# Optimization experiments

Measured on AMD Instinct MI355X. Metric: run time of the kernel, lower is better.

## Reference

```python
import jax, jax.numpy as jnp
import numpy as np


def _unfold(x, k):
    # x: [B, C, H, W] -> [B, C, S, L] with S=k*k (row-major patch order), L=H*W
    B, C, H, W = x.shape
    pad = k // 2
    xp = jnp.pad(x, ((0, 0), (0, 0), (pad, pad), (pad, pad)))
    patches = jnp.stack(
        [xp[:, :, r:r + H, c:c + W] for r in range(k) for c in range(k)], axis=2
    )  # [B, C, S, H, W]
    return patches.reshape(B, C, k * k, H * W)


def setup_inputs() -> dict:
    key = jax.random.key(0)
    ks = jax.random.split(key, 8)
    B, C, H, W = 8, 64, 128, 128
    R, Cout = 4, 128
    x = jax.random.normal(ks[0], (B, C, H, W), dtype=jnp.float32)
    gate_w = jax.random.normal(ks[1], (R, C), dtype=jnp.float32) * 0.05   # 1x1 gate conv weight
    gate_b = jax.random.normal(ks[2], (R,), dtype=jnp.float32) * 0.01
    theta = jax.random.normal(ks[3], (R,), dtype=jnp.float32) * 0.5       # learned directions
    raw_sigma_u = jax.random.normal(ks[4], (R,), dtype=jnp.float32) * 0.1
    raw_sigma_s = jax.random.normal(ks[5], (R,), dtype=jnp.float32) * 0.1
    pw_w = jax.random.normal(ks[6], (Cout, R * C), dtype=jnp.float32) * (1.0 / np.sqrt(R * C).astype(np.float32))
    pw_b = jax.random.normal(ks[7], (Cout,), dtype=jnp.float32) * 0.01
    return {"x": x, "gate_w": gate_w, "gate_b": gate_b, "theta": theta,
            "raw_sigma_u": raw_sigma_u, "raw_sigma_s": raw_sigma_s,
            "pw_w": pw_w, "pw_b": pw_b}


def reference(x, gate_w, gate_b, theta, raw_sigma_u, raw_sigma_s, pw_w, pw_b):
    k = 3
    B, C, H, W = x.shape
    R = theta.shape[0]
    S, L = k * k, H * W

    x_un = _unfold(x, k)                                         # [B, C, S, L]

    # 1x1 gate conv + fuzzy softmax over rules
    logits = jnp.einsum('bchw,rc->brhw', x, gate_w) + gate_b[None, :, None, None]
    mu = jax.nn.softmax(logits, axis=1)                          # [B, R, H, W]
    mu_un = _unfold(mu, k)                                       # [B, R, S, L]
    s_center = (k // 2) * k + (k // 2)
    mu_center = mu_un[:, :, s_center:s_center + 1, :]            # [B, R, 1, L]

    # anisotropic Gaussian kernel per rule over integer offsets (row-major)
    grid = np.arange(k, dtype=np.float32) - k // 2
    dy = jnp.asarray(np.repeat(grid, k))                         # [S]
    dx = jnp.asarray(np.tile(grid, k))                           # [S]
    cos_t, sin_t = jnp.cos(theta)[:, None], jnp.sin(theta)[:, None]
    proj_u = cos_t * dx[None, :] + sin_t * dy[None, :]           # [R, S]
    proj_s = -sin_t * dx[None, :] + cos_t * dy[None, :]
    su = (jax.nn.softplus(raw_sigma_u) + 1e-4)[:, None]
    ss = (jax.nn.softplus(raw_sigma_s) + 1e-4)[:, None]
    kern = jnp.exp(-proj_u ** 2 / su ** 2 - proj_s ** 2 / ss ** 2)  # [R, S]

    alpha = mu_center * mu_un * kern[None, :, :, None]           # [B, R, S, L]
    alpha_sum = jnp.maximum(alpha.sum(axis=(1, 2), keepdims=True), 1e-8)
    alpha = alpha / alpha_sum

    agg = jnp.einsum('brsl,bcsl->brcl', alpha, x_un)             # [B, R, C, L]
    agg_flat = agg.reshape(B, R * C, L)
    out = jnp.einsum('bnl,on->bol', agg_flat, pw_w) + pw_b[None, :, None]
    return out.reshape(B, -1, H, W)
```

## Files before the change

kernel.cpp:

```cpp
#include <hip/hip_runtime.h>
#include <math.h>

#define CC 64
#define RR 4
#define HH 128
#define WW 128
#define BB 8
#define COUT 128
#define XST 72
#define ALS 44

typedef __attribute__((ext_vector_type(8))) short short8;
typedef __attribute__((ext_vector_type(4))) float f32x4;
typedef __attribute__((ext_vector_type(2))) float f32x2;

__device__ __forceinline__ unsigned short f2bf(float f) {
  unsigned u = __float_as_uint(f);
  u += 0x7fffu + ((u >> 16) & 1u);
  return (unsigned short)(u >> 16);
}
__device__ __forceinline__ float blo(unsigned u) { return __uint_as_float(u << 16); }
__device__ __forceinline__ float bhi(unsigned u) { return __uint_as_float(u & 0xffff0000u); }
__device__ __forceinline__ int swzx(int cb, int sp) { return cb ^ ((sp >> 3) & 7); }
__device__ __forceinline__ int swza(int cb, int row) { return cb ^ ((row >> 3) & 3); }

__global__ __launch_bounds__(256) void k_pre(const float* __restrict__ theta,
                                             const float* __restrict__ rsu,
                                             const float* __restrict__ rss,
                                             const float* __restrict__ pw,
                                             const float* __restrict__ gw,
                                             float* __restrict__ wkern,
                                             unsigned short* __restrict__ pwb,
                                             unsigned short* __restrict__ gwb) {
  int i = blockIdx.x * 256 + threadIdx.x;
  if (i < COUT * RR * CC) pwb[i] = f2bf(pw[i]);
  if (blockIdx.x == 0 && threadIdx.x < RR * 9) {
    int t = threadIdx.x;
    int r = t / 9, s = t % 9;
    float dy = (float)(s / 3 - 1), dx = (float)(s % 3 - 1);
    float ct = cosf(theta[r]), st = sinf(theta[r]);
    float su = log1pf(expf(rsu[r])) + 1e-4f;
    float sv = log1pf(expf(rss[r])) + 1e-4f;
    float pu = ct * dx + st * dy;
    float ps = -st * dx + ct * dy;
    wkern[t] = expf(-(pu * pu) / (su * su) - (ps * ps) / (sv * sv));
  }
  if (blockIdx.x == 1) {
    #pragma unroll
    for (int k = 0; k < 4; ++k) {
      int j = k * 256 + threadIdx.x;
      gwb[j] = (j < RR * CC) ? f2bf(gw[j]) : (unsigned short)0;
    }
  }
}

__global__ __launch_bounds__(256, 3) void k_fused(const float* __restrict__ x,
                                                  const float* __restrict__ gb,
                                                  const float* __restrict__ wkern,
                                                  const unsigned short* __restrict__ pwb,
                                                  const unsigned short* __restrict__ gwb,
                                                  const float* __restrict__ pb,
                                                  float* __restrict__ out) {
  __shared__ unsigned short xsT[160][XST];
  __shared__ float mus[RR][4][40];
  __shared__ unsigned short alp[64][ALS];
  __shared__ float rsum[RR][64];
  __shared__ __align__(16) unsigned short aggs[32][264];

  int tid = threadIdx.x;
  int raw = blockIdx.x;
  int bid = (raw & 7) * 256 + (raw >> 3);
  int b = bid >> 8;
  int rem = bid & 255;
  int h0 = (rem >> 2) << 1;
  int w0 = (rem & 3) << 5;

  int lane = tid & 63;
  int wv = tid >> 6;
  int lr = lane & 15, lq = lane >> 4;
  int o0 = wv << 5;

  short8 a0r[8], a1r[8];
  {
    const unsigned short* pA = pwb + ((o0 + lr) << 8) + (lq << 3);
    #pragma unroll
    for (int ks = 0; ks < 8; ++ks) {
      a0r[ks] = *(const short8*)(pA + (ks << 5));
      a1r[ks] = *(const short8*)(pA + 4096 + (ks << 5));
    }
  }
  short8 am0 = *(const short8*)(gwb + (lr << 6) + (lq << 3));
  short8 am1 = *(const short8*)(gwb + (lr << 6) + 32 + (lq << 3));
  float4 pbv0 = *(const float4*)&pb[o0 + (lq << 2)];
  float4 pbv1 = *(const float4*)&pb[o0 + 16 + (lq << 2)];
  float gb0 = gb[0], gb1 = gb[1], gb2 = gb[2], gb3 = gb[3];

  #pragma unroll
  for (int k = 0; k < 3; ++k) {
    int item = k * 256 + tid;
    if (item < 640) {
      int c4 = item % 10;
      int rest = item / 10;
      int row = rest & 3, cquad = rest >> 2;
      int c = cquad << 2;
      int gcol = w0 - 4 + (c4 << 2);
      int grow = h0 - 1 + row;
      float4 v0 = make_float4(0.f,0.f,0.f,0.f), v1 = v0, v2 = v0, v3 = v0;
      if ((unsigned)gcol < WW && (unsigned)grow < HH) {
        const float* xp = x + (((size_t)b * CC + c) << 14) + (grow << 7) + gcol;
        v0 = *(const float4*)xp;
        v1 = *(const float4*)(xp + (1 << 14));
        v2 = *(const float4*)(xp + (2 << 14));
        v3 = *(const float4*)(xp + (3 << 14));
      }
      int spb = row * 40 + (c4 << 2);
      int cb = cquad >> 1, sub = (cquad & 1) << 2;
      float4 vv[4] = {v0, v1, v2, v3};
      #pragma unroll
      for (int j = 0; j < 4; ++j) {
        int sp = spb + j;
        ushort4 uv;
        uv.x = f2bf(vv[0].x); uv.y = f2bf(vv[1].x); uv.z = f2bf(vv[2].x); uv.w = f2bf(vv[3].x);
        float f0 = (&vv[0].x)[j], f1 = (&vv[1].x)[j], f2v = (&vv[2].x)[j], f3 = (&vv[3].x)[j];
        uv.x = f2bf(f0); uv.y = f2bf(f1); uv.z = f2bf(f2v); uv.w = f2bf(f3);
        *(ushort4*)&xsT[sp][(swzx(cb, sp) << 3) + sub] = uv;
      }
    }
  }
  __syncthreads();

  for (int j = wv; j < 9; j += 4) {
    int p = (j << 4) + lr;
    int pcl = p > 135 ? 135 : p;
    unsigned y = (unsigned)pcl / 34u;
    int cxo = pcl - (int)(y * 34u);
    int pos = (int)y * 40 + 3 + cxo;
    short8 b0 = *(const short8*)&xsT[pos][swzx(lq, pos) << 3];
    short8 b1 = *(const short8*)&xsT[pos][swzx(4 + lq, pos) << 3];
    f32x4 mac = (f32x4){0.f, 0.f, 0.f, 0.f};
    mac = __builtin_amdgcn_mfma_f32_16x16x32_bf16(am0, b0, mac, 0, 0, 0);
    mac = __builtin_amdgcn_mfma_f32_16x16x32_bf16(am1, b1, mac, 0, 0, 0);
    if (lq == 0 && p < 136) {
      int grow = h0 - 1 + (int)y, gcol = w0 - 1 + cxo;
      float lg0 = mac[0] + gb0, lg1 = mac[1] + gb1;
      float lg2 = mac[2] + gb2, lg3 = mac[3] + gb3;
      float m = fmaxf(fmaxf(lg0, lg1), fmaxf(lg2, lg3));
      float e0 = expf(lg0 - m), e1 = expf(lg1 - m);
      float e2 = expf(lg2 - m), e3 = expf(lg3 - m);
      float inv = 1.0f / (e0 + e1 + e2 + e3);
      if (!((unsigned)grow < HH && (unsigned)gcol < WW)) inv = 0.0f;
      mus[0][y][3 + cxo] = e0 * inv;
      mus[1][y][3 + cxo] = e1 * inv;
      mus[2][y][3 + cxo] = e2 * inv;
      mus[3][y][3 + cxo] = e3 * inv;
    }
  }
  __syncthreads();

  {
    int t = tid & 63, r = tid >> 6;
    int prow = t >> 5, pcol = t & 31;
    float mc = mus[r][prow + 1][pcol + 4];
    float sum = 0.f;
    #pragma unroll
    for (int s = 0; s < 9; ++s) {
      float av = mc * mus[r][prow + s / 3][pcol + 3 + s % 3] * wkern[r * 9 + s];
      alp[t][(s << 2) + r] = f2bf(av);
      sum += av;
    }
    rsum[r][t] = sum;
  }
  __syncthreads();

  #pragma unroll
  for (int p = 0; p < 2; ++p) {
    {
      int t = tid & 31, cg = tid >> 5;
      int px = (p << 5) + t;
      float inv = 1.0f / fmaxf(rsum[0][px] + rsum[1][px] + rsum[2][px] + rsum[3][px], 1e-8f);

      uint2 ad[9];
      #pragma unroll
      for (int s = 0; s < 9; ++s) ad[s] = *(const uint2*)(&alp[px][s << 2]);

      f32x2 cacc[4][4];
      #pragma unroll
      for (int r = 0; r < 4; ++r)
        #pragma unroll
        for (int j = 0; j < 4; ++j) cacc[r][j] = (f32x2){0.f, 0.f};

      #pragma unroll
      for (int s = 0; s < 9; ++s) {
        int sp = (p + s / 3) * 40 + t + 3 + s % 3;
        uint4 ux = *(const uint4*)&xsT[sp][swzx(cg, sp) << 3];
        f32x2 xv0 = {blo(ux.x), bhi(ux.x)};
        f32x2 xv1 = {blo(ux.y), bhi(ux.y)};
        f32x2 xv2 = {blo(ux.z), bhi(ux.z)};
        f32x2 xv3 = {blo(ux.w), bhi(ux.w)};
        unsigned adx = ad[s].x, ady = ad[s].y;
        float af0 = blo(adx), af1 = bhi(adx), af2 = blo(ady), af3 = bhi(ady);
        f32x2 A0 = {af0, af0}, A1 = {af1, af1}, A2 = {af2, af2}, A3 = {af3, af3};
        cacc[0][0] += A0 * xv0; cacc[0][1] += A0 * xv1; cacc[0][2] += A0 * xv2; cacc[0][3] += A0 * xv3;
        cacc[1][0] += A1 * xv0; cacc[1][1] += A1 * xv1; cacc[1][2] += A1 * xv2; cacc[1][3] += A1 * xv3;
        cacc[2][0] += A2 * xv0; cacc[2][1] += A2 * xv1; cacc[2][2] += A2 * xv2; cacc[2][3] += A2 * xv3;
        cacc[3][0] += A3 * xv0; cacc[3][1] += A3 * xv1; cacc[3][2] += A3 * xv2; cacc[3][3] += A3 * xv3;
      }
      #pragma unroll
      for (int r = 0; r < 4; ++r) {
        short8 wvv;
        #pragma unroll
        for (int j = 0; j < 4; ++j) {
          wvv[2 * j]     = (short)f2bf(cacc[r][j][0] * inv);
          wvv[2 * j + 1] = (short)f2bf(cacc[r][j][1] * inv);
        }
        *(short8*)&aggs[t][swza((r << 3) + cg, t) << 3] = wvv;
      }
    }
    __syncthreads();

    f32x4 dacc[2][2];
    #pragma unroll
    for (int i = 0; i < 2; ++i)
      #pragma unroll
      for (int j = 0; j < 2; ++j) dacc[i][j] = (f32x4){0.f, 0.f, 0.f, 0.f};

    #pragma unroll
    for (int ks = 0; ks < 8; ++ks) {
      short8 b0 = *(const short8*)&aggs[lr][swza((ks << 2) + lq, lr) << 3];
      short8 b1 = *(const short8*)&aggs[16 + lr][swza((ks << 2) + lq, 16 + lr) << 3];
      dacc[0][0] = __builtin_amdgcn_mfma_f32_16x16x32_bf16(a0r[ks], b0, dacc[0][0], 0, 0, 0);
      dacc[0][1] = __builtin_amdgcn_mfma_f32_16x16x32_bf16(a0r[ks], b1, dacc[0][1], 0, 0, 0);
      dacc[1][0] = __builtin_amdgcn_mfma_f32_16x16x32_bf16(a1r[ks], b0, dacc[1][0], 0, 0, 0);
      dacc[1][1] = __builtin_amdgcn_mfma_f32_16x16x32_bf16(a1r[ks], b1, dacc[1][1], 0, 0, 0);
    }

    #pragma unroll
    for (int oi = 0; oi < 2; ++oi) {
      float4 pbv = oi ? pbv1 : pbv0;
      #pragma unroll
      for (int q = 0; q < 4; ++q) {
        int o = o0 + (oi << 4) + (lq << 2) + q;
        size_t base = (((size_t)b * COUT + o) << 14) + ((h0 + p) << 7) + w0;
        out[base + lr]      = dacc[oi][0][q] + pbv[q];
        out[base + 16 + lr] = dacc[oi][1][q] + pbv[q];
      }
    }
    if (p == 0) __syncthreads();
  }
}

extern "C" void kernel_launch(void* const* d_in, const int* in_sizes, int n_in,
                              void* d_out, int out_size, void* d_ws, size_t ws_size,
                              hipStream_t stream) {
  const float* x     = (const float*)d_in[0];
  const float* gw    = (const float*)d_in[1];
  const float* gb    = (const float*)d_in[2];
  const float* theta = (const float*)d_in[3];
  const float* rsu   = (const float*)d_in[4];
  const float* rss   = (const float*)d_in[5];
  const float* pw    = (const float*)d_in[6];
  const float* pb    = (const float*)d_in[7];
  float* outp = (float*)d_out;

  float* wkern = (float*)d_ws;
  unsigned short* pwb = (unsigned short*)(wkern + 64);
  unsigned short* gwb = pwb + COUT * RR * CC;

  k_pre<<<128, 256, 0, stream>>>(theta, rsu, rss, pw, gw, wkern, pwb, gwb);
  k_fused<<<BB * (HH / 2) * (WW / 32), 256, 0, stream>>>(x, gb, wkern, pwb, gwb, pb, outp);
}
```

Baseline: 51.10 us.

## Split aggregation into four 16-pixel rounds and shrink LDS buffers

Restructures the aggregation and pointwise stage from two 32-pixel passes into four 16-pixel rounds. Each thread now accumulates 4 channels instead of 8, and the MFMA accumulators are held across round pairs before the output is written. The gate softmax values are stored as bf16 and the aggs buffer is halved, which reduces shared memory and registers, likely to allow more blocks per CU. The cost is extra barriers, less MFMA work per barrier, and slightly lower precision for mu.

```diff
diff --git a/kernel.cpp b/kernel.cpp
--- a/kernel.cpp
+++ b/kernel.cpp
@@ -18,6 +18,9 @@
   unsigned u = __float_as_uint(f);
   u += 0x7fffu + ((u >> 16) & 1u);
   return (unsigned short)(u >> 16);
+}
+__device__ __forceinline__ float bf2f(unsigned short h) {
+  return __uint_as_float(((unsigned)h) << 16);
 }
 __device__ __forceinline__ float blo(unsigned u) { return __uint_as_float(u << 16); }
 __device__ __forceinline__ float bhi(unsigned u) { return __uint_as_float(u & 0xffff0000u); }
@@ -62,10 +65,10 @@
                                                   const float* __restrict__ pb,
                                                   float* __restrict__ out) {
   __shared__ unsigned short xsT[160][XST];
-  __shared__ float mus[RR][4][40];
+  __shared__ unsigned short mus[RR][4][40];
   __shared__ unsigned short alp[64][ALS];
   __shared__ float rsum[RR][64];
-  __shared__ __align__(16) unsigned short aggs[32][264];
+  __shared__ __align__(16) unsigned short aggs[16][264];
 
   int tid = threadIdx.x;
   int raw = blockIdx.x;
@@ -119,9 +122,8 @@
       #pragma unroll
       for (int j = 0; j < 4; ++j) {
         int sp = spb + j;
+        float f0 = (&vv[0].x)[j], f1 = (&vv[1].x)[j], f2v = (&vv[2].x)[j], f3 = (&vv[3].x)[j];
         ushort4 uv;
-        uv.x = f2bf(vv[0].x); uv.y = f2bf(vv[1].x); uv.z = f2bf(vv[2].x); uv.w = f2bf(vv[3].x);
-        float f0 = (&vv[0].x)[j], f1 = (&vv[1].x)[j], f2v = (&vv[2].x)[j], f3 = (&vv[3].x)[j];
         uv.x = f2bf(f0); uv.y = f2bf(f1); uv.z = f2bf(f2v); uv.w = f2bf(f3);
         *(ushort4*)&xsT[sp][(swzx(cb, sp) << 3) + sub] = uv;
       }
@@ -149,10 +151,10 @@
       float e2 = expf(lg2 - m), e3 = expf(lg3 - m);
       float inv = 1.0f / (e0 + e1 + e2 + e3);
       if (!((unsigned)grow < HH && (unsigned)gcol < WW)) inv = 0.0f;
-      mus[0][y][3 + cxo] = e0 * inv;
-      mus[1][y][3 + cxo] = e1 * inv;
-      mus[2][y][3 + cxo] = e2 * inv;
-      mus[3][y][3 + cxo] = e3 * inv;
+      mus[0][y][3 + cxo] = f2bf(e0 * inv);
+      mus[1][y][3 + cxo] = f2bf(e1 * inv);
+      mus[2][y][3 + cxo] = f2bf(e2 * inv);
+      mus[3][y][3 + cxo] = f2bf(e3 * inv);
     }
   }
   __syncthreads();
@@ -160,11 +162,11 @@
   {
     int t = tid & 63, r = tid >> 6;
     int prow = t >> 5, pcol = t & 31;
-    float mc = mus[r][prow + 1][pcol + 4];
+    float mc = bf2f(mus[r][prow + 1][pcol + 4]);
     float sum = 0.f;
     #pragma unroll
     for (int s = 0; s < 9; ++s) {
-      float av = mc * mus[r][prow + s / 3][pcol + 3 + s % 3] * wkern[r * 9 + s];
+      float av = mc * bf2f(mus[r][prow + s / 3][pcol + 3 + s % 3]) * wkern[r * 9 + s];
       alp[t][(s << 2) + r] = f2bf(av);
       sum += av;
     }
@@ -172,80 +174,79 @@
   }
   __syncthreads();
 
+  f32x4 dprev0 = (f32x4){0.f, 0.f, 0.f, 0.f};
+  f32x4 dprev1 = (f32x4){0.f, 0.f, 0.f, 0.f};
   #pragma unroll
-  for (int p = 0; p < 2; ++p) {
+  for (int rd = 0; rd < 4; ++rd) {
     {
-      int t = tid & 31, cg = tid >> 5;
-      int px = (p << 5) + t;
+      int t16 = tid & 15, cg = tid >> 4;
+      int px = (rd << 4) + t16;
+      int prow2 = px >> 5, pc = px & 31;
       float inv = 1.0f / fmaxf(rsum[0][px] + rsum[1][px] + rsum[2][px] + rsum[3][px], 1e-8f);
 
       uint2 ad[9];
       #pragma unroll
       for (int s = 0; s < 9; ++s) ad[s] = *(const uint2*)(&alp[px][s << 2]);
 
-      f32x2 cacc[4][4];
-      #pragma unroll
-      for (int r = 0; r < 4; ++r)
-        #pragma unroll
-        for (int j = 0; j < 4; ++j) cacc[r][j] = (f32x2){0.f, 0.f};
-
+      f32x2 cacc[4][2];
+      #pragma unroll
+      for (int r = 0; r < 4; ++r) {
+        cacc[r][0] = (f32x2){0.f, 0.f};
+        cacc[r][1] = (f32x2){0.f, 0.f};
+      }
+
+      int cb = cg >> 1, sub = (cg & 1) << 2;
       #pragma unroll
       for (int s = 0; s < 9; ++s) {
-        int sp = (p + s / 3) * 40 + t + 3 + s % 3;
-        uint4 ux = *(const uint4*)&xsT[sp][swzx(cg, sp) << 3];
+        int sp = (prow2 + s / 3) * 40 + pc + 3 + s % 3;
+        uint2 ux = *(const uint2*)&xsT[sp][(swzx(cb, sp) << 3) + sub];
         f32x2 xv0 = {blo(ux.x), bhi(ux.x)};
         f32x2 xv1 = {blo(ux.y), bhi(ux.y)};
-        f32x2 xv2 = {blo(ux.z), bhi(ux.z)};
-        f32x2 xv3 = {blo(ux.w), bhi(ux.w)};
         unsigned adx = ad[s].x, ady = ad[s].y;
         float af0 = blo(adx), af1 = bhi(adx), af2 = blo(ady), af3 = bhi(ady);
         f32x2 A0 = {af0, af0}, A1 = {af1, af1}, A2 = {af2, af2}, A3 = {af3, af3};
-        cacc[0][0] += A0 * xv0; cacc[0][1] += A0 * xv1; cacc[0][2] += A0 * xv2; cacc[0][3] += A0 * xv3;
-        cacc[1][0] += A1 * xv0; cacc[1][1] += A1 * xv1; cacc[1][2] += A1 * xv2; cacc[1][3] += A1 * xv3;
-        cacc[2][0] += A2 * xv0; cacc[2][1] += A2 * xv1; cacc[2][2] += A2 * xv2; cacc[2][3] += A2 * xv3;
-        cacc[3][0] += A3 * xv0; cacc[3][1] += A3 * xv1; cacc[3][2] += A3 * xv2; cacc[3][3] += A3 * xv3;
+        cacc[0][0] += A0 * xv0; cacc[0][1] += A0 * xv1;
+        cacc[1][0] += A1 * xv0; cacc[1][1] += A1 * xv1;
+        cacc[2][0] += A2 * xv0; cacc[2][1] += A2 * xv1;
+        cacc[3][0] += A3 * xv0; cacc[3][1] += A3 * xv1;
       }
       #pragma unroll
       for (int r = 0; r < 4; ++r) {
-        short8 wvv;
+        ushort4 wvv;
+        wvv.x = f2bf(cacc[r][0][0] * inv); wvv.y = f2bf(cacc[r][0][1] * inv);
+        wvv.z = f2bf(cacc[r][1][0] * inv); wvv.w = f2bf(cacc[r][1][1] * inv);
+        int kb = (r << 3) + cb;
+        *(ushort4*)&aggs[t16][(swza(kb, t16) << 3) + sub] = wvv;
+      }
+    }
+    __syncthreads();
+
+    {
+      f32x4 dacc0 = (f32x4){0.f, 0.f, 0.f, 0.f};
+      f32x4 dacc1 = (f32x4){0.f, 0.f, 0.f, 0.f};
+      #pragma unroll
+      for (int ks = 0; ks < 8; ++ks) {
+        short8 b0 = *(const short8*)&aggs[lr][swza((ks << 2) + lq, lr) << 3];
+        dacc0 = __builtin_amdgcn_mfma_f32_16x16x32_bf16(a0r[ks], b0, dacc0, 0, 0, 0);
+        dacc1 = __builtin_amdgcn_mfma_f32_16x16x32_bf16(a1r[ks], b0, dacc1, 0, 0, 0);
+      }
+      if ((rd & 1) == 0) {
+        dprev0 = dacc0; dprev1 = dacc1;
+      } else {
+        int orow = h0 + (rd >> 1);
         #pragma unroll
-        for (int j = 0; j < 4; ++j) {
-          wvv[2 * j]     = (short)f2bf(cacc[r][j][0] * inv);
-          wvv[2 * j + 1] = (short)f2bf(cacc[r][j][1] * inv);
+        for (int q = 0; q < 4; ++q) {
+          int o = o0 + (lq << 2) + q;
+          size_t base0 = (((size_t)b * COUT + o) << 14) + (orow << 7) + w0;
+          size_t base1 = (((size_t)b * COUT + o + 16) << 14) + (orow << 7) + w0;
+          out[base0 + lr]      = dprev0[q] + pbv0[q];
+          out[base0 + 16 + lr] = dacc0[q] + pbv0[q];
+          out[base1 + lr]      = dprev1[q] + pbv1[q];
+          out[base1 + 16 + lr] = dacc1[q] + pbv1[q];
         }
-        *(short8*)&aggs[t][swza((r << 3) + cg, t) << 3] = wvv;
-      }
-    }
-    __syncthreads();
-
-    f32x4 dacc[2][2];
-    #pragma unroll
-    for (int i = 0; i < 2; ++i)
-      #pragma unroll
-      for (int j = 0; j < 2; ++j) dacc[i][j] = (f32x4){0.f, 0.f, 0.f, 0.f};
-
-    #pragma unroll
-    for (int ks = 0; ks < 8; ++ks) {
-      short8 b0 = *(const short8*)&aggs[lr][swza((ks << 2) + lq, lr) << 3];
-      short8 b1 = *(const short8*)&aggs[16 + lr][swza((ks << 2) + lq, 16 + lr) << 3];
-      dacc[0][0] = __builtin_amdgcn_mfma_f32_16x16x32_bf16(a0r[ks], b0, dacc[0][0], 0, 0, 0);
-      dacc[0][1] = __builtin_amdgcn_mfma_f32_16x16x32_bf16(a0r[ks], b1, dacc[0][1], 0, 0, 0);
-      dacc[1][0] = __builtin_amdgcn_mfma_f32_16x16x32_bf16(a1r[ks], b0, dacc[1][0], 0, 0, 0);
-      dacc[1][1] = __builtin_amdgcn_mfma_f32_16x16x32_bf16(a1r[ks], b1, dacc[1][1], 0, 0, 0);
-    }
-
-    #pragma unroll
-    for (int oi = 0; oi < 2; ++oi) {
-      float4 pbv = oi ? pbv1 : pbv0;
-      #pragma unroll
-      for (int q = 0; q < 4; ++q) {
-        int o = o0 + (oi << 4) + (lq << 2) + q;
-        size_t base = (((size_t)b * COUT + o) << 14) + ((h0 + p) << 7) + w0;
-        out[base + lr]      = dacc[oi][0][q] + pbv[q];
-        out[base + 16 + lr] = dacc[oi][1][q] + pbv[q];
-      }
-    }
-    if (p == 0) __syncthreads();
+      }
+    }
+    if (rd < 3) __syncthreads();
   }
 }
 
```

New measurement: 54.38 us. 1.06x slower.
